# Kernel optimization log

Measured on AMD Instinct MI355X. Metric: run time of the kernel, lower is better.

## Reference

```python
import jax, jax.numpy as jnp
import numpy as np
from jax import lax

GEN_POLY = ("1111001", "1011011")  # rate 1/2, constraint length 7 (octal 171/133)


def build_trellis(gen_poly):
    """Feed-forward (non-recursive) convolutional trellis tables.

    State = shift-register contents, most-recent bit is the MSB of the state
    index. Returns int32 tables, each [ns, ni]:
      to_nodes[s, b]        : next state from state s with input bit b
      op_by_fromnode[s, b]  : emitted output-symbol index for (s, b)
      from_nodes[j, m]      : m-th predecessor state of state j
      ip_by_tonode[j, m]    : input bit taken on that predecessor transition
    """
    mu = len(gen_poly[0]) - 1
    ns, ni = 2 ** mu, 2
    g = np.array([[int(c) for c in p] for p in gen_poly])  # [conv_n, mu+1]
    to_nodes = np.zeros((ns, ni), np.int32)
    op_by_fromnode = np.zeros((ns, ni), np.int32)
    from_nodes = np.zeros((ns, ni), np.int32)
    ip_by_tonode = np.zeros((ns, ni), np.int32)
    fill = np.zeros(ns, np.int32)
    for s in range(ns):
        rbits = [(s >> (mu - 1 - j)) & 1 for j in range(mu)]
        for b in range(ni):
            w = np.array([b] + rbits)                 # full window [b, r0..r_{mu-1}]
            obits = (g @ w) % 2                        # output bits, MSB first
            o = int("".join(str(int(x)) for x in obits), 2)
            j = int("".join(str(x) for x in ([b] + rbits[:-1])), 2)
            to_nodes[s, b] = j
            op_by_fromnode[s, b] = o
            from_nodes[j, fill[j]] = s
            ip_by_tonode[j, fill[j]] = b
            fill[j] += 1
    return to_nodes, op_by_fromnode, from_nodes, ip_by_tonode


TO_NODES, OP_BY_FROM, FROM_NODES, IP_BY_TO = build_trellis(GEN_POLY)
CONV_N = len(GEN_POLY)
MU = len(GEN_POLY[0]) - 1
NS = 2 ** MU
NO = 2 ** CONV_N
# output-symbol bit patterns, MSB first, mapped to signs (1-2*bit)
_OP_BITS = np.array([[(o >> (CONV_N - 1 - j)) & 1 for j in range(CONV_N)]
                     for o in range(NO)], np.float32)
OP_SIGN = jnp.asarray(1.0 - 2.0 * _OP_BITS)  # [NO, CONV_N]
IP_SIGN = jnp.asarray([1.0, -1.0])           # sign of input bit b: 1-2b


def setup_inputs() -> dict:
    key = jax.random.key(0)
    k1, k2 = jax.random.split(key)
    B, n = 256, 4096
    T = n // CONV_N  # = k = 2048 info bits
    llr_ch = jax.random.normal(k1, (B, n), dtype=jnp.float32)
    llr_a = jax.random.normal(k2, (B, T), dtype=jnp.float32)
    return {"llr_ch": llr_ch, "llr_a": llr_a}


def _bcjr(llr_ch, llr_a):
    B, n = llr_ch.shape
    T = n // CONV_N
    # branch metrics: bm[t, b, o] = exp(0.5 * sum_j llr[b, t, j] * (1-2*opbit_j(o)))
    llr_r = llr_ch.reshape(B, T, CONV_N)
    bm = jnp.exp(0.5 * jnp.einsum('btj,oj->tbo', llr_r, OP_SIGN))  # [T, B, NO]
    llr_a_t = llr_a.T  # [T, B]

    def gamma_fn(bm_t, la_t):
        # a-priori factor exp(0.5*llr_a*(1-2b)) times channel branch metric
        ap = jnp.exp(0.5 * la_t[:, None, None] * IP_SIGN[None, None, :])  # [B,1,2]
        return ap * bm_t[:, OP_BY_FROM]  # [B, NS, 2]

    alpha0 = jnp.zeros((B, NS), jnp.float32).at[:, 0].set(1.0)

    def fwd(alpha_prev, inp):
        bm_t, la_t = inp
        gam = gamma_fn(bm_t, la_t)                        # [B, NS, 2] by from-state
        ag = gam * alpha_prev[:, :, None]                  # alpha_{t} * gamma_t
        agt = ag[:, FROM_NODES, IP_BY_TO]                  # regroup by to-state
        alpha = agt.sum(-1)
        alpha = alpha / alpha.sum(-1, keepdims=True)       # normalize (as in TF code)
        return alpha, alpha_prev                            # emit alpha BEFORE step t

    _, alphas = lax.scan(fwd, alpha0, (bm, llr_a_t))       # alphas[t] = alpha_t, [T,B,NS]

    beta_T = jnp.full((B, NS), 1.0 / NS, jnp.float32)      # non-terminated: uniform

    def bwd(beta_next, inp):
        bm_t, la_t, alpha_t = inp
        gam = gamma_fn(bm_t, la_t)                         # [B, NS, 2]
        bg = gam * beta_next[:, TO_NODES]                  # gamma * beta_{t+1}(to)
        beta = bg.sum(-1)
        beta = beta / beta.sum(-1, keepdims=True)
        joint = alpha_t[:, :, None] * bg                   # APP per (state, bit)
        llr_t = jnp.log(joint[..., 0].sum(-1)) - jnp.log(joint[..., 1].sum(-1))
        return beta, llr_t

    _, llrs_rev = lax.scan(bwd, beta_T, (bm[::-1], llr_a_t[::-1], alphas[::-1]))
    return llrs_rev[::-1].T  # [B, T] soft LLRs (hard_out=False)


def reference(llr_ch, llr_a):
    return _bcjr(llr_ch, llr_a)
```

## Files before the change

kernel.cpp:

```cpp
#include <hip/hip_runtime.h>

#define T_LEN 2048
#define NSTATE 64
#define NCHUNK 32
#define CH_S 64
#define HF 32
#define WARM 48
#define RK 16
#define ROWQ 20

template<int CTRL>
__device__ __forceinline__ float dpp_add(float v) {
    int r = __builtin_amdgcn_update_dpp(0, __float_as_int(v), CTRL, 0xF, 0xF, true);
    return v + __int_as_float(r);
}

__device__ __forceinline__ float dpp_mov_xor1(float v) {
    return __int_as_float(__builtin_amdgcn_update_dpp(0, __float_as_int(v), 0xB1, 0xF, 0xF, true));
}

__device__ __forceinline__ float dpp_sum_to63(float v) {
    v = dpp_add<0x111>(v);
    v = dpp_add<0x112>(v);
    v = dpp_add<0x114>(v);
    v = dpp_add<0x118>(v);
    v = dpp_add<0x142>(v);
    v = dpp_add<0x143>(v);
    return v;
}

__device__ __forceinline__ float wave_total(float v) {
    float s = dpp_sum_to63(v);
    return __int_as_float(__builtin_amdgcn_readlane(__float_as_int(s), 63));
}

__device__ __forceinline__ float pair_sum_xor1(float v) {
    int r = __builtin_amdgcn_update_dpp(0, __float_as_int(v), 0xB1, 0xF, 0xF, true);
    return v + __int_as_float(r);
}

__device__ __forceinline__ float bperm(int addrb, float v) {
    return __int_as_float(__builtin_amdgcn_ds_bpermute(addrb, __float_as_int(v)));
}

__device__ __forceinline__ unsigned bf16_of(float f) {
    return (__float_as_uint(f) + 0x8000u) >> 16;
}
template<int HI>
__device__ __forceinline__ float bf16_half(unsigned w) {
    return __uint_as_float(HI ? (w & 0xffff0000u) : (w << 16));
}

__device__ __forceinline__ float stash63(float acc, float v, int L, int lane) {
    float bc = __int_as_float(__builtin_amdgcn_readlane(__float_as_int(v), 63));
    return (lane == L) ? bc : acc;
}


template<int MODE>
__device__ __forceinline__ float fwd_group(float state,
                                           const float* __restrict__ chp,
                                           const float* __restrict__ lap,
                                           unsigned* __restrict__ alds,
                                           const unsigned* __restrict__ blds,
                                           float* __restrict__ outp,
                                           int g, int t0, int lane,
                                           float kE, float k0, float k1,
                                           int fselb)
{
    float acc = 1.0f;
    #pragma unroll
    for (int h = 0; h < 2; ++h) {
        const int gb = g + 8 * h;
        const float4* c4 = (const float4*)(chp + 2 * gb);
        const float4* a4 = (const float4*)(lap + gb);
        float4 cc[4], aa[2];
        #pragma unroll
        for (int i = 0; i < 4; ++i) cc[i] = c4[i];
        #pragma unroll
        for (int i = 0; i < 2; ++i) aa[i] = a4[i];
        uint4 bw0, bw1;
        if (MODE == 2) {
            const int off = (gb - t0 - HF) >> 1;
            bw0 = *(const uint4*)(blds + (lane >> 1) * ROWQ + off);
            bw1 = *(const uint4*)(blds + (32 + (lane >> 1)) * ROWQ + off);
        }
        unsigned pk[4];
        #pragma unroll
        for (int i = 0; i < 8; ++i) {
            float l0 = (i & 1) ? cc[i >> 1].z : cc[i >> 1].x;
            float l1 = (i & 1) ? cc[i >> 1].w : cc[i >> 1].y;
            float la = ((const float*)aa)[i];
            if (MODE == 1) {
                unsigned hs = bf16_of(state);
                if (i & 1) pk[i >> 1] |= hs << 16; else pk[i >> 1] = hs;
            }
            float x   = fmaf(la, kE, fmaf(l0, k0, l1 * k1));
            float g0v = exp2f(x);
            float g1v = __builtin_amdgcn_rcpf(g0v);
            float sg0 = state * g0v;
            float sg1 = state * g1v;
            if (MODE == 2) {
                unsigned w0 = (&bw0.x)[i >> 1];
                unsigned w1 = (&bw1.x)[i >> 1];
                float b0v = (i & 1) ? bf16_half<1>(w0) : bf16_half<0>(w0);
                float b1v = (i & 1) ? bf16_half<1>(w1) : bf16_half<0>(w1);
                float na = dpp_sum_to63(sg0 * b0v);
                float nb = dpp_sum_to63(sg1 * b1v);
                acc = stash63(acc, na, 2 * (8 * h + i), lane);
                acc = stash63(acc, nb, 2 * (8 * h + i) + 1, lane);
            }
            float s0 = pair_sum_xor1(sg0);
            float s1 = pair_sum_xor1(sg1);
            float v  = (lane & 1) ? s1 : s0;
            state = bperm(fselb, v);
        }
        if (MODE == 1)
            *(uint4*)(alds + lane * ROWQ + ((gb - t0) >> 1)) =
                make_uint4(pk[0], pk[1], pk[2], pk[3]);
    }
    if (MODE == 2) {
        float lg = __log2f(acc);
        float dl = (lg - dpp_mov_xor1(lg)) * 0.6931471805599453f;
        if (lane < 32 && !(lane & 1)) outp[g + (lane >> 1)] = dl;
    }
    float s = wave_total(state);
    return state * __builtin_amdgcn_rcpf(s);
}

template<int MODE>
__device__ __forceinline__ float bwd_group(float state,
                                           const float* __restrict__ chp,
                                           const float* __restrict__ lap,
                                           const unsigned* __restrict__ alds,
                                           unsigned* __restrict__ blds,
                                           float* __restrict__ outp,
                                           int g, int t0, int lane,
                                           float kE, float k0, float k1,
                                           unsigned pmask, int bgb)
{
    const bool odd = (lane & 1);
    float acc = 1.0f;
    #pragma unroll
    for (int h = 1; h >= 0; --h) {
        const int gb = g + 8 * h;
        const float4* c4 = (const float4*)(chp + 2 * gb);
        const float4* a4 = (const float4*)(lap + gb);
        float4 cc[4], aa[2];
        #pragma unroll
        for (int i = 0; i < 4; ++i) cc[i] = c4[i];
        #pragma unroll
        for (int i = 0; i < 2; ++i) aa[i] = a4[i];
        uint4 aw;
        if (MODE == 2)
            aw = *(const uint4*)(alds + lane * ROWQ + ((gb - t0) >> 1));
        unsigned pk[4];
        #pragma unroll
        for (int i = 7; i >= 0; --i) {
            float l0 = (i & 1) ? cc[i >> 1].z : cc[i >> 1].x;
            float l1 = (i & 1) ? cc[i >> 1].w : cc[i >> 1].y;
            float la = ((const float*)aa)[i];
            if (MODE == 1) {
                unsigned hs = bf16_of(state);
                if (i & 1) pk[i >> 1] = hs << 16; else pk[i >> 1] |= hs;
            }
            float x  = fmaf(la, kE, fmaf(l0, k0, l1 * k1));
            float xg = __uint_as_float(__float_as_uint(x) ^ pmask);
            float ga  = exp2f(xg);
            float gb_ = __builtin_amdgcn_rcpf(ga);
            float a  = bperm(bgb, state);
            float bb = dpp_mov_xor1(a);
            float u0 = ga * a;
            float u1 = gb_ * bb;
            if (MODE == 2) {
                unsigned w = (&aw.x)[i >> 1];
                float av = (i & 1) ? bf16_half<1>(w) : bf16_half<0>(w);
                float ua = odd ? u1 : u0;
                float ub = odd ? u0 : u1;
                float na = dpp_sum_to63(av * ua);
                float nb = dpp_sum_to63(av * ub);
                acc = stash63(acc, na, 2 * (8 * h + i), lane);
                acc = stash63(acc, nb, 2 * (8 * h + i) + 1, lane);
            }
            state = u0 + u1;
        }
        if (MODE == 1)
            *(uint4*)(blds + lane * ROWQ + ((gb - t0 - HF) >> 1)) =
                make_uint4(pk[0], pk[1], pk[2], pk[3]);
    }
    if (MODE == 2) {
        float lg = __log2f(acc);
        float dl = (lg - dpp_mov_xor1(lg)) * 0.6931471805599453f;
        if (lane < 32 && !(lane & 1)) outp[g + (lane >> 1)] = dl;
    }
    float s = wave_total(state);
    return state * __builtin_amdgcn_rcpf(s);
}

__global__ __launch_bounds__(128, 8)
void bcjr_fused_kernel(const float* __restrict__ llr_ch,
                       const float* __restrict__ llr_a,
                       float* __restrict__ out)
{
    __shared__ __align__(16) unsigned alds[NSTATE * ROWQ];
    __shared__ __align__(16) unsigned blds[NSTATE * ROWQ];

    const int lane  = threadIdx.x & 63;
    const int role  = threadIdx.x >> 6;
    const int unit  = blockIdx.x;
    const int chunk = unit & (NCHUNK - 1);
    const int b     = unit >> 5;

    const float c0 = 1.0f - 2.0f * (float)(__popc(lane & 57) & 1);
    const float c1 = 1.0f - 2.0f * (float)(__popc(lane & 27) & 1);
    const float kE = 0.5f * 1.442695040888963f;
    const float k0 = kE * c0, k1 = kE * c1;

    const float* chp = llr_ch + (size_t)b * (2 * T_LEN);
    const float* lap = llr_a  + (size_t)b * T_LEN;
    float* outp = out + (size_t)b * T_LEN;
    const int t0 = chunk * CH_S;

    if (role == 0) {
        const int fselb = (2 * (lane & 31) + (lane >> 5)) << 2;
        float state = (chunk == 0) ? ((lane == 0) ? 1.0f : 0.0f) : (1.0f / 64.0f);
        const int ts = (chunk == 0) ? t0 : t0 - WARM;
        for (int g = ts; g < t0; g += RK)
            state = fwd_group<0>(state, chp, lap, alds, blds, outp, g, t0, lane, kE, k0, k1, fselb);
        for (int g = t0; g < t0 + HF; g += RK)
            state = fwd_group<1>(state, chp, lap, alds, blds, outp, g, t0, lane, kE, k0, k1, fselb);
        __syncthreads();
        for (int g = t0 + HF; g < t0 + CH_S; g += RK)
            state = fwd_group<2>(state, chp, lap, alds, blds, outp, g, t0, lane, kE, k0, k1, fselb);
    } else {
        const unsigned pmask = (unsigned)(lane & 1) << 31;
        const int bgb = ((lane >> 1) + ((lane & 1) << 5)) << 2;
        float state = 1.0f / 64.0f;
        const int te = (chunk == NCHUNK - 1) ? (t0 + CH_S) : (t0 + CH_S + WARM);
        for (int g = te - RK; g >= t0 + CH_S; g -= RK)
            state = bwd_group<0>(state, chp, lap, alds, blds, outp, g, t0, lane, kE, k0, k1, pmask, bgb);
        for (int g = t0 + CH_S - RK; g >= t0 + HF; g -= RK)
            state = bwd_group<1>(state, chp, lap, alds, blds, outp, g, t0, lane, kE, k0, k1, pmask, bgb);
        __syncthreads();
        for (int g = t0 + HF - RK; g >= t0; g -= RK)
            state = bwd_group<2>(state, chp, lap, alds, blds, outp, g, t0, lane, kE, k0, k1, pmask, bgb);
    }
}

extern "C" void kernel_launch(void* const* d_in, const int* in_sizes, int n_in,
                              void* d_out, int out_size, void* d_ws, size_t ws_size,
                              hipStream_t stream) {
    const float* llr_ch = (const float*)d_in[0];
    const float* llr_a  = (const float*)d_in[1];
    float* out = (float*)d_out;

    int B = in_sizes[0] / (2 * T_LEN);
    (void)d_ws; (void)ws_size;

    int n_units = B * NCHUNK;
    hipLaunchKernelGGL(bcjr_fused_kernel, dim3(n_units), dim3(128), 0, stream,
                       llr_ch, llr_a, out);
}
```

Baseline: 136.4 us.

## Process two batch rows per wave to interleave independent trellis recursions

Each block now handles two batch elements, and each wave runs two independent forward or backward recursions interleaved step by step. The goal is to fill the latency of the serial DPP, bpermute and transcendental dependency chains with independent work from the second trajectory. In exchange, LDS per block doubles, register pressure rises, launch bounds drop to 4 blocks per SM, and the grid is halved. The launch now assumes an even batch size.

```diff
diff --git a/kernel.cpp b/kernel.cpp
--- a/kernel.cpp
+++ b/kernel.cpp
@@ -8,6 +8,7 @@
 #define WARM 48
 #define RK 16
 #define ROWQ 20
+#define TRAJ (NSTATE * ROWQ)
 
 template<int CTRL>
 __device__ __forceinline__ float dpp_add(float v) {
@@ -58,192 +59,308 @@
 
 
 template<int MODE>
-__device__ __forceinline__ float fwd_group(float state,
-                                           const float* __restrict__ chp,
-                                           const float* __restrict__ lap,
+__device__ __forceinline__ void fwd_group2(float& sA, float& sB,
+                                           const float* __restrict__ chpA,
+                                           const float* __restrict__ chpB,
+                                           const float* __restrict__ lapA,
+                                           const float* __restrict__ lapB,
                                            unsigned* __restrict__ alds,
                                            const unsigned* __restrict__ blds,
-                                           float* __restrict__ outp,
+                                           float* __restrict__ outA,
+                                           float* __restrict__ outB,
                                            int g, int t0, int lane,
                                            float kE, float k0, float k1,
                                            int fselb)
 {
-    float acc = 1.0f;
+    float accA = 1.0f, accB = 1.0f;
     #pragma unroll
     for (int h = 0; h < 2; ++h) {
         const int gb = g + 8 * h;
-        const float4* c4 = (const float4*)(chp + 2 * gb);
-        const float4* a4 = (const float4*)(lap + gb);
-        float4 cc[4], aa[2];
-        #pragma unroll
-        for (int i = 0; i < 4; ++i) cc[i] = c4[i];
-        #pragma unroll
-        for (int i = 0; i < 2; ++i) aa[i] = a4[i];
-        uint4 bw0, bw1;
+        float4 ccA[4], aaA[2], ccB[4], aaB[2];
+        {
+            const float4* c4 = (const float4*)(chpA + 2 * gb);
+            const float4* a4 = (const float4*)(lapA + gb);
+            #pragma unroll
+            for (int i = 0; i < 4; ++i) ccA[i] = c4[i];
+            #pragma unroll
+            for (int i = 0; i < 2; ++i) aaA[i] = a4[i];
+        }
+        {
+            const float4* c4 = (const float4*)(chpB + 2 * gb);
+            const float4* a4 = (const float4*)(lapB + gb);
+            #pragma unroll
+            for (int i = 0; i < 4; ++i) ccB[i] = c4[i];
+            #pragma unroll
+            for (int i = 0; i < 2; ++i) aaB[i] = a4[i];
+        }
+        uint4 bw0A, bw1A, bw0B, bw1B;
         if (MODE == 2) {
             const int off = (gb - t0 - HF) >> 1;
-            bw0 = *(const uint4*)(blds + (lane >> 1) * ROWQ + off);
-            bw1 = *(const uint4*)(blds + (32 + (lane >> 1)) * ROWQ + off);
-        }
-        unsigned pk[4];
+            bw0A = *(const uint4*)(blds + (lane >> 1) * ROWQ + off);
+            bw1A = *(const uint4*)(blds + (32 + (lane >> 1)) * ROWQ + off);
+            bw0B = *(const uint4*)(blds + TRAJ + (lane >> 1) * ROWQ + off);
+            bw1B = *(const uint4*)(blds + TRAJ + (32 + (lane >> 1)) * ROWQ + off);
+        }
+        unsigned pkA[4], pkB[4];
         #pragma unroll
         for (int i = 0; i < 8; ++i) {
-            float l0 = (i & 1) ? cc[i >> 1].z : cc[i >> 1].x;
-            float l1 = (i & 1) ? cc[i >> 1].w : cc[i >> 1].y;
-            float la = ((const float*)aa)[i];
-            if (MODE == 1) {
-                unsigned hs = bf16_of(state);
-                if (i & 1) pk[i >> 1] |= hs << 16; else pk[i >> 1] = hs;
+            {
+                float l0 = (i & 1) ? ccA[i >> 1].z : ccA[i >> 1].x;
+                float l1 = (i & 1) ? ccA[i >> 1].w : ccA[i >> 1].y;
+                float la = ((const float*)aaA)[i];
+                if (MODE == 1) {
+                    unsigned hs = bf16_of(sA);
+                    if (i & 1) pkA[i >> 1] |= hs << 16; else pkA[i >> 1] = hs;
+                }
+                float x   = fmaf(la, kE, fmaf(l0, k0, l1 * k1));
+                float g0v = exp2f(x);
+                float g1v = __builtin_amdgcn_rcpf(g0v);
+                float sg0 = sA * g0v;
+                float sg1 = sA * g1v;
+                if (MODE == 2) {
+                    unsigned w0 = (&bw0A.x)[i >> 1];
+                    unsigned w1 = (&bw1A.x)[i >> 1];
+                    float b0v = (i & 1) ? bf16_half<1>(w0) : bf16_half<0>(w0);
+                    float b1v = (i & 1) ? bf16_half<1>(w1) : bf16_half<0>(w1);
+                    float na = dpp_sum_to63(sg0 * b0v);
+                    float nb = dpp_sum_to63(sg1 * b1v);
+                    accA = stash63(accA, na, 2 * (8 * h + i), lane);
+                    accA = stash63(accA, nb, 2 * (8 * h + i) + 1, lane);
+                }
+                float s0 = pair_sum_xor1(sg0);
+                float s1 = pair_sum_xor1(sg1);
+                float v  = (lane & 1) ? s1 : s0;
+                sA = bperm(fselb, v);
             }
-            float x   = fmaf(la, kE, fmaf(l0, k0, l1 * k1));
-            float g0v = exp2f(x);
-            float g1v = __builtin_amdgcn_rcpf(g0v);
-            float sg0 = state * g0v;
-            float sg1 = state * g1v;
-            if (MODE == 2) {
-                unsigned w0 = (&bw0.x)[i >> 1];
-                unsigned w1 = (&bw1.x)[i >> 1];
-                float b0v = (i & 1) ? bf16_half<1>(w0) : bf16_half<0>(w0);
-                float b1v = (i & 1) ? bf16_half<1>(w1) : bf16_half<0>(w1);
-                float na = dpp_sum_to63(sg0 * b0v);
-                float nb = dpp_sum_to63(sg1 * b1v);
-                acc = stash63(acc, na, 2 * (8 * h + i), lane);
-                acc = stash63(acc, nb, 2 * (8 * h + i) + 1, lane);
+            {
+                float l0 = (i & 1) ? ccB[i >> 1].z : ccB[i >> 1].x;
+                float l1 = (i & 1) ? ccB[i >> 1].w : ccB[i >> 1].y;
+                float la = ((const float*)aaB)[i];
+                if (MODE == 1) {
+                    unsigned hs = bf16_of(sB);
+                    if (i & 1) pkB[i >> 1] |= hs << 16; else pkB[i >> 1] = hs;
+                }
+                float x   = fmaf(la, kE, fmaf(l0, k0, l1 * k1));
+                float g0v = exp2f(x);
+                float g1v = __builtin_amdgcn_rcpf(g0v);
+                float sg0 = sB * g0v;
+                float sg1 = sB * g1v;
+                if (MODE == 2) {
+                    unsigned w0 = (&bw0B.x)[i >> 1];
+                    unsigned w1 = (&bw1B.x)[i >> 1];
+                    float b0v = (i & 1) ? bf16_half<1>(w0) : bf16_half<0>(w0);
+                    float b1v = (i & 1) ? bf16_half<1>(w1) : bf16_half<0>(w1);
+                    float na = dpp_sum_to63(sg0 * b0v);
+                    float nb = dpp_sum_to63(sg1 * b1v);
+                    accB = stash63(accB, na, 2 * (8 * h + i), lane);
+                    accB = stash63(accB, nb, 2 * (8 * h + i) + 1, lane);
+                }
+                float s0 = pair_sum_xor1(sg0);
+                float s1 = pair_sum_xor1(sg1);
+                float v  = (lane & 1) ? s1 : s0;
+                sB = bperm(fselb, v);
             }
-            float s0 = pair_sum_xor1(sg0);
-            float s1 = pair_sum_xor1(sg1);
-            float v  = (lane & 1) ? s1 : s0;
-            state = bperm(fselb, v);
-        }
-        if (MODE == 1)
+        }
+        if (MODE == 1) {
             *(uint4*)(alds + lane * ROWQ + ((gb - t0) >> 1)) =
-                make_uint4(pk[0], pk[1], pk[2], pk[3]);
+                make_uint4(pkA[0], pkA[1], pkA[2], pkA[3]);
+            *(uint4*)(alds + TRAJ + lane * ROWQ + ((gb - t0) >> 1)) =
+                make_uint4(pkB[0], pkB[1], pkB[2], pkB[3]);
+        }
     }
     if (MODE == 2) {
-        float lg = __log2f(acc);
-        float dl = (lg - dpp_mov_xor1(lg)) * 0.6931471805599453f;
-        if (lane < 32 && !(lane & 1)) outp[g + (lane >> 1)] = dl;
-    }
-    float s = wave_total(state);
-    return state * __builtin_amdgcn_rcpf(s);
+        float lgA = __log2f(accA);
+        float dlA = (lgA - dpp_mov_xor1(lgA)) * 0.6931471805599453f;
+        float lgB = __log2f(accB);
+        float dlB = (lgB - dpp_mov_xor1(lgB)) * 0.6931471805599453f;
+        if (lane < 32 && !(lane & 1)) {
+            outA[g + (lane >> 1)] = dlA;
+            outB[g + (lane >> 1)] = dlB;
+        }
+    }
+    float tA = wave_total(sA);
+    sA = sA * __builtin_amdgcn_rcpf(tA);
+    float tB = wave_total(sB);
+    sB = sB * __builtin_amdgcn_rcpf(tB);
 }
 
 template<int MODE>
-__device__ __forceinline__ float bwd_group(float state,
-                                           const float* __restrict__ chp,
-                                           const float* __restrict__ lap,
+__device__ __forceinline__ void bwd_group2(float& sA, float& sB,
+                                           const float* __restrict__ chpA,
+                                           const float* __restrict__ chpB,
+                                           const float* __restrict__ lapA,
+                                           const float* __restrict__ lapB,
                                            const unsigned* __restrict__ alds,
                                            unsigned* __restrict__ blds,
-                                           float* __restrict__ outp,
+                                           float* __restrict__ outA,
+                                           float* __restrict__ outB,
                                            int g, int t0, int lane,
                                            float kE, float k0, float k1,
                                            unsigned pmask, int bgb)
 {
     const bool odd = (lane & 1);
-    float acc = 1.0f;
+    float accA = 1.0f, accB = 1.0f;
     #pragma unroll
     for (int h = 1; h >= 0; --h) {
         const int gb = g + 8 * h;
-        const float4* c4 = (const float4*)(chp + 2 * gb);
-        const float4* a4 = (const float4*)(lap + gb);
-        float4 cc[4], aa[2];
-        #pragma unroll
-        for (int i = 0; i < 4; ++i) cc[i] = c4[i];
-        #pragma unroll
-        for (int i = 0; i < 2; ++i) aa[i] = a4[i];
-        uint4 aw;
-        if (MODE == 2)
-            aw = *(const uint4*)(alds + lane * ROWQ + ((gb - t0) >> 1));
-        unsigned pk[4];
+        float4 ccA[4], aaA[2], ccB[4], aaB[2];
+        {
+            const float4* c4 = (const float4*)(chpA + 2 * gb);
+            const float4* a4 = (const float4*)(lapA + gb);
+            #pragma unroll
+            for (int i = 0; i < 4; ++i) ccA[i] = c4[i];
+            #pragma unroll
+            for (int i = 0; i < 2; ++i) aaA[i] = a4[i];
+        }
+        {
+            const float4* c4 = (const float4*)(chpB + 2 * gb);
+            const float4* a4 = (const float4*)(lapB + gb);
+            #pragma unroll
+            for (int i = 0; i < 4; ++i) ccB[i] = c4[i];
+            #pragma unroll
+            for (int i = 0; i < 2; ++i) aaB[i] = a4[i];
+        }
+        uint4 awA, awB;
+        if (MODE == 2) {
+            awA = *(const uint4*)(alds + lane * ROWQ + ((gb - t0) >> 1));
+            awB = *(const uint4*)(alds + TRAJ + lane * ROWQ + ((gb - t0) >> 1));
+        }
+        unsigned pkA[4], pkB[4];
         #pragma unroll
         for (int i = 7; i >= 0; --i) {
-            float l0 = (i & 1) ? cc[i >> 1].z : cc[i >> 1].x;
-            float l1 = (i & 1) ? cc[i >> 1].w : cc[i >> 1].y;
-            float la = ((const float*)aa)[i];
-            if (MODE == 1) {
-                unsigned hs = bf16_of(state);
-                if (i & 1) pk[i >> 1] = hs << 16; else pk[i >> 1] |= hs;
+            {
+                float l0 = (i & 1) ? ccA[i >> 1].z : ccA[i >> 1].x;
+                float l1 = (i & 1) ? ccA[i >> 1].w : ccA[i >> 1].y;
+                float la = ((const float*)aaA)[i];
+                if (MODE == 1) {
+                    unsigned hs = bf16_of(sA);
+                    if (i & 1) pkA[i >> 1] = hs << 16; else pkA[i >> 1] |= hs;
+                }
+                float x  = fmaf(la, kE, fmaf(l0, k0, l1 * k1));
+                float xg = __uint_as_float(__float_as_uint(x) ^ pmask);
+                float ga  = exp2f(xg);
+                float gb_ = __builtin_amdgcn_rcpf(ga);
+                float a  = bperm(bgb, sA);
+                float bb = dpp_mov_xor1(a);
+                float u0 = ga * a;
+                float u1 = gb_ * bb;
+                if (MODE == 2) {
+                    unsigned w = (&awA.x)[i >> 1];
+                    float av = (i & 1) ? bf16_half<1>(w) : bf16_half<0>(w);
+                    float ua = odd ? u1 : u0;
+                    float ub = odd ? u0 : u1;
+                    float na = dpp_sum_to63(av * ua);
+                    float nb = dpp_sum_to63(av * ub);
+                    accA = stash63(accA, na, 2 * (8 * h + i), lane);
+                    accA = stash63(accA, nb, 2 * (8 * h + i) + 1, lane);
+                }
+                sA = u0 + u1;
             }
-            float x  = fmaf(la, kE, fmaf(l0, k0, l1 * k1));
-            float xg = __uint_as_float(__float_as_uint(x) ^ pmask);
-            float ga  = exp2f(xg);
-            float gb_ = __builtin_amdgcn_rcpf(ga);
-            float a  = bperm(bgb, state);
-            float bb = dpp_mov_xor1(a);
-            float u0 = ga * a;
-            float u1 = gb_ * bb;
-            if (MODE == 2) {
-                unsigned w = (&aw.x)[i >> 1];
-                float av = (i & 1) ? bf16_half<1>(w) : bf16_half<0>(w);
-                float ua = odd ? u1 : u0;
-                float ub = odd ? u0 : u1;
-                float na = dpp_sum_to63(av * ua);
-                float nb = dpp_sum_to63(av * ub);
-                acc = stash63(acc, na, 2 * (8 * h + i), lane);
-                acc = stash63(acc, nb, 2 * (8 * h + i) + 1, lane);
+            {
+                float l0 = (i & 1) ? ccB[i >> 1].z : ccB[i >> 1].x;
+                float l1 = (i & 1) ? ccB[i >> 1].w : ccB[i >> 1].y;
+                float la = ((const float*)aaB)[i];
+                if (MODE == 1) {
+                    unsigned hs = bf16_of(sB);
+                    if (i & 1) pkB[i >> 1] = hs << 16; else pkB[i >> 1] |= hs;
+                }
+                float x  = fmaf(la, kE, fmaf(l0, k0, l1 * k1));
+                float xg = __uint_as_float(__float_as_uint(x) ^ pmask);
+                float ga  = exp2f(xg);
+                float gb_ = __builtin_amdgcn_rcpf(ga);
+                float a  = bperm(bgb, sB);
+                float bb = dpp_mov_xor1(a);
+                float u0 = ga * a;
+                float u1 = gb_ * bb;
+                if (MODE == 2) {
+                    unsigned w = (&awB.x)[i >> 1];
+                    float av = (i & 1) ? bf16_half<1>(w) : bf16_half<0>(w);
+                    float ua = odd ? u1 : u0;
+                    float ub = odd ? u0 : u1;
+                    float na = dpp_sum_to63(av * ua);
+                    float nb = dpp_sum_to63(av * ub);
+                    accB = stash63(accB, na, 2 * (8 * h + i), lane);
+                    accB = stash63(accB, nb, 2 * (8 * h + i) + 1, lane);
+                }
+                sB = u0 + u1;
             }
-            state = u0 + u1;
-        }
-        if (MODE == 1)
+        }
+        if (MODE == 1) {
             *(uint4*)(blds + lane * ROWQ + ((gb - t0 - HF) >> 1)) =
-                make_uint4(pk[0], pk[1], pk[2], pk[3]);
+                make_uint4(pkA[0], pkA[1], pkA[2], pkA[3]);
+            *(uint4*)(blds + TRAJ + lane * ROWQ + ((gb - t0 - HF) >> 1)) =
+                make_uint4(pkB[0], pkB[1], pkB[2], pkB[3]);
+        }
     }
     if (MODE == 2) {
-        float lg = __log2f(acc);
-        float dl = (lg - dpp_mov_xor1(lg)) * 0.6931471805599453f;
-        if (lane < 32 && !(lane & 1)) outp[g + (lane >> 1)] = dl;
-    }
-    float s = wave_total(state);
-    return state * __builtin_amdgcn_rcpf(s);
-}
-
-__global__ __launch_bounds__(128, 8)
+        float lgA = __log2f(accA);
+        float dlA = (lgA - dpp_mov_xor1(lgA)) * 0.6931471805599453f;
+        float lgB = __log2f(accB);
+        float dlB = (lgB - dpp_mov_xor1(lgB)) * 0.6931471805599453f;
+        if (lane < 32 && !(lane & 1)) {
+            outA[g + (lane >> 1)] = dlA;
+            outB[g + (lane >> 1)] = dlB;
+        }
+    }
+    float tA = wave_total(sA);
+    sA = sA * __builtin_amdgcn_rcpf(tA);
+    float tB = wave_total(sB);
+    sB = sB * __builtin_amdgcn_rcpf(tB);
+}
+
+__global__ __launch_bounds__(128, 4)
 void bcjr_fused_kernel(const float* __restrict__ llr_ch,
                        const float* __restrict__ llr_a,
                        float* __restrict__ out)
 {
-    __shared__ __align__(16) unsigned alds[NSTATE * ROWQ];
-    __shared__ __align__(16) unsigned blds[NSTATE * ROWQ];
+    __shared__ __align__(16) unsigned alds[2 * TRAJ];
+    __shared__ __align__(16) unsigned blds[2 * TRAJ];
 
     const int lane  = threadIdx.x & 63;
     const int role  = threadIdx.x >> 6;
     const int unit  = blockIdx.x;
     const int chunk = unit & (NCHUNK - 1);
-    const int b     = unit >> 5;
+    const int bp    = unit >> 5;
+    const int bA    = 2 * bp;
+    const int bB    = 2 * bp + 1;
 
     const float c0 = 1.0f - 2.0f * (float)(__popc(lane & 57) & 1);
     const float c1 = 1.0f - 2.0f * (float)(__popc(lane & 27) & 1);
     const float kE = 0.5f * 1.442695040888963f;
     const float k0 = kE * c0, k1 = kE * c1;
 
-    const float* chp = llr_ch + (size_t)b * (2 * T_LEN);
-    const float* lap = llr_a  + (size_t)b * T_LEN;
-    float* outp = out + (size_t)b * T_LEN;
+    const float* chpA = llr_ch + (size_t)bA * (2 * T_LEN);
+    const float* chpB = llr_ch + (size_t)bB * (2 * T_LEN);
+    const float* lapA = llr_a  + (size_t)bA * T_LEN;
+    const float* lapB = llr_a  + (size_t)bB * T_LEN;
+    float* outA = out + (size_t)bA * T_LEN;
+    float* outB = out + (size_t)bB * T_LEN;
     const int t0 = chunk * CH_S;
 
     if (role == 0) {
         const int fselb = (2 * (lane & 31) + (lane >> 5)) << 2;
-        float state = (chunk == 0) ? ((lane == 0) ? 1.0f : 0.0f) : (1.0f / 64.0f);
+        float init = (chunk == 0) ? ((lane == 0) ? 1.0f : 0.0f) : (1.0f / 64.0f);
+        float sA = init, sB = init;
         const int ts = (chunk == 0) ? t0 : t0 - WARM;
         for (int g = ts; g < t0; g += RK)
-            state = fwd_group<0>(state, chp, lap, alds, blds, outp, g, t0, lane, kE, k0, k1, fselb);
+            fwd_group2<0>(sA, sB, chpA, chpB, lapA, lapB, alds, blds, outA, outB, g, t0, lane, kE, k0, k1, fselb);
         for (int g = t0; g < t0 + HF; g += RK)
-            state = fwd_group<1>(state, chp, lap, alds, blds, outp, g, t0, lane, kE, k0, k1, fselb);
+            fwd_group2<1>(sA, sB, chpA, chpB, lapA, lapB, alds, blds, outA, outB, g, t0, lane, kE, k0, k1, fselb);
         __syncthreads();
         for (int g = t0 + HF; g < t0 + CH_S; g += RK)
-            state = fwd_group<2>(state, chp, lap, alds, blds, outp, g, t0, lane, kE, k0, k1, fselb);
+            fwd_group2<2>(sA, sB, chpA, chpB, lapA, lapB, alds, blds, outA, outB, g, t0, lane, kE, k0, k1, fselb);
     } else {
         const unsigned pmask = (unsigned)(lane & 1) << 31;
         const int bgb = ((lane >> 1) + ((lane & 1) << 5)) << 2;
-        float state = 1.0f / 64.0f;
+        float sA = 1.0f / 64.0f, sB = 1.0f / 64.0f;
         const int te = (chunk == NCHUNK - 1) ? (t0 + CH_S) : (t0 + CH_S + WARM);
         for (int g = te - RK; g >= t0 + CH_S; g -= RK)
-            state = bwd_group<0>(state, chp, lap, alds, blds, outp, g, t0, lane, kE, k0, k1, pmask, bgb);
+            bwd_group2<0>(sA, sB, chpA, chpB, lapA, lapB, alds, blds, outA, outB, g, t0, lane, kE, k0, k1, pmask, bgb);
         for (int g = t0 + CH_S - RK; g >= t0 + HF; g -= RK)
-            state = bwd_group<1>(state, chp, lap, alds, blds, outp, g, t0, lane, kE, k0, k1, pmask, bgb);
+            bwd_group2<1>(sA, sB, chpA, chpB, lapA, lapB, alds, blds, outA, outB, g, t0, lane, kE, k0, k1, pmask, bgb);
         __syncthreads();
         for (int g = t0 + HF - RK; g >= t0; g -= RK)
-            state = bwd_group<2>(state, chp, lap, alds, blds, outp, g, t0, lane, kE, k0, k1, pmask, bgb);
+            bwd_group2<2>(sA, sB, chpA, chpB, lapA, lapB, alds, blds, outA, outB, g, t0, lane, kE, k0, k1, pmask, bgb);
     }
 }
 
@@ -257,7 +374,7 @@
     int B = in_sizes[0] / (2 * T_LEN);
     (void)d_ws; (void)ws_size;
 
-    int n_units = B * NCHUNK;
+    int n_units = (B / 2) * NCHUNK;
     hipLaunchKernelGGL(bcjr_fused_kernel, dim3(n_units), dim3(128), 0, stream,
                        llr_ch, llr_a, out);
 }
```

After: 140.9 us. 3.3% more time.
